# Kernel tuning notes

Measured on AMD Instinct MI355X. Metric: run time of the kernel, lower is better.

The kernel has to match this reference:

```python
import jax, jax.numpy as jnp
import numpy as np

DIM = 128      # d_msa
HEADS = 8
DH = 64        # dim_head
INNER = HEADS * DH  # 512
R = 64         # tie_attn_dim (MSA rows)
N = 512        # residues
DPAIR = 128
LN_EPS = 1e-5


def _layernorm(x, g, b):
    mu = jnp.mean(x, axis=-1, keepdims=True)
    var = jnp.mean((x - mu) ** 2, axis=-1, keepdims=True)
    return (x - mu) * jax.lax.rsqrt(var + LN_EPS) * g + b


def setup_inputs() -> dict:
    key = jax.random.key(0)
    ks = jax.random.split(key, 12)
    s = 0.02
    return {
        "x": jax.random.normal(ks[0], (R, N, DIM), jnp.float32),
        "pair_bias": jax.random.normal(ks[1], (1, N, N, DPAIR), jnp.float32),
        "Wq": jax.random.normal(ks[2], (DIM, INNER), jnp.float32) * s,
        "Wkv": jax.random.normal(ks[3], (DIM, 2 * INNER), jnp.float32) * s,
        "Wo": jax.random.normal(ks[4], (INNER, DIM), jnp.float32) * s,
        "bo": jnp.zeros((DIM,), jnp.float32),
        "ln_g": jnp.ones((DPAIR,), jnp.float32),
        "ln_b": jnp.zeros((DPAIR,), jnp.float32),
        "Wpair": jax.random.normal(ks[5], (DPAIR, HEADS), jnp.float32) * s,
        "Wsq": jax.random.normal(ks[6], (DIM, DIM), jnp.float32) * s,
        "bsq": jnp.zeros((DIM,), jnp.float32),
        "Wsk": jax.random.normal(ks[7], (DIM, DIM), jnp.float32) * s,
        "bsk": jnp.zeros((DIM,), jnp.float32),
        "tie_attn_dim": R,
    }


def reference(x, pair_bias, Wq, Wkv, Wo, bo, ln_g, ln_b, Wpair, Wsq, bsq, Wsk, bsk, tie_attn_dim):
    r = tie_attn_dim
    br, n, dim = x.shape
    b = br // r
    h, dh = HEADS, DH
    dsw = dim // h  # per-head dim inside PositionalWiseWeight

    # projections: (b*r, n, inner) -> (b, r, h, n, dh)
    q = (x @ Wq).reshape(b, r, n, h, dh).transpose(0, 1, 3, 2, 4)
    kv = x @ Wkv
    k, v = jnp.split(kv, 2, axis=-1)
    k = k.reshape(b, r, n, h, dh).transpose(0, 1, 3, 2, 4)
    v = v.reshape(b, r, n, h, dh).transpose(0, 1, 3, 2, 4)

    # soft tied row weights (PositionalWiseWeight): w[b, i(pos), h, r]
    m = x.reshape(b, r, n, dim)
    sq = (m[:, :1] @ Wsq + bsq).reshape(b, 1, n, h, dsw).transpose(0, 2, 3, 1, 4)  # b n h 1 d
    sk = (m @ Wsk + bsk).reshape(b, r, n, h, dsw).transpose(0, 2, 3, 1, 4)          # b n h r d
    wlog = jnp.einsum('bnhud,bnhrd->bnhr', sq, sk) / np.float32(np.sqrt(dsw))
    w = jax.nn.softmax(wlog, axis=-1)  # softmax over rows r

    # tied-row attention logits with soft weights
    scale = np.float32(dh) ** -0.5
    dots = jnp.einsum('bihr,brhid,brhjd->bhij', w, q, k) * scale

    # pair bias: LayerNorm + Linear(dim_pair -> heads), broadcast into logits
    pb = _layernorm(pair_bias, ln_g, ln_b) @ Wpair  # (b, i, j, h)
    dots = dots + pb.transpose(0, 3, 1, 2)

    attn = jax.nn.softmax(dots, axis=-1)  # (b, h, i, j)

    out = jnp.einsum('bhij,brhjd->brhid', attn, v)           # (b, r, h, n, dh)
    out = out.transpose(0, 1, 3, 2, 4).reshape(br, n, h * dh)
    out = out @ Wo + bo                                       # (b*r, n, dim)
    return out.reshape(1, br, n, dim)
```

## Files before the change

### kernel.cpp

```cpp
#include <hip/hip_runtime.h>
#include <hip/hip_bf16.h>

typedef unsigned short u16;
typedef unsigned int u32;
typedef __attribute__((ext_vector_type(8))) short short8;
typedef __attribute__((ext_vector_type(4))) float floatx4;

__device__ inline float bf2f(u16 u) { union { u32 i; float f; } v; v.i = ((u32)u) << 16; return v.f; }
__device__ inline u16 f2bf(float f) {
    union { float f; u32 i; } v; v.f = f;
    u32 lsb = (v.i >> 16) & 1u;
    v.i += 0x7fffu + lsb;
    return (u16)(v.i >> 16);
}

__device__ inline void ld8(u16* dst, const float* src) {
    const float4 a = *(const float4*)src;
    const float4 b = *(const float4*)(src + 4);
    uint4 q;
    q.x = (u32)f2bf(a.x) | ((u32)f2bf(a.y) << 16);
    q.y = (u32)f2bf(a.z) | ((u32)f2bf(a.w) << 16);
    q.z = (u32)f2bf(b.x) | ((u32)f2bf(b.y) << 16);
    q.w = (u32)f2bf(b.z) | ((u32)f2bf(b.w) << 16);
    *(uint4*)dst = q;
}

__device__ inline void async16(u16* ldst, const u16* gsrc) {
    __builtin_amdgcn_global_load_lds((const __attribute__((address_space(1))) u32*)gsrc,
                                     (__attribute__((address_space(3))) u32*)ldst, 16, 0, 0);
}

template <int BM, int BN, class Epi>
__global__ __launch_bounds__(256) void gemm_nt(const u16* __restrict__ A, const u16* __restrict__ B,
                                               long sAz, long sBz, int lda, int ldb, int K, int zlog, Epi epi)
{
    constexpr int AELE = BM * 32, BELE = BN * 32;
    constexpr int IA = BM / 64, IB = BN / 64;
    __shared__ __align__(16) u16 lds[2 * (AELE + BELE)];
    const int tid  = threadIdx.x;
    const int lane = tid & 63;
    const int wave = tid >> 6;
    const int z    = blockIdx.z;
    const int zh   = z >> zlog;
    const int zk   = z & ((1 << zlog) - 1);
    const long row0 = (long)blockIdx.y * BM;
    const long col0 = (long)blockIdx.x * BN;
    const u16* Ab = A + (long)zh * sAz + row0 * lda + (long)zk * K;
    const u16* Bb = B + (long)zh * sBz + col0 * ldb + (long)zk * K;
    constexpr int WM = BM / 2, WN = BN / 2, TM = WM / 16, TN = WN / 16;
    const int wm = (wave >> 1) * WM;
    const int wn = (wave & 1) * WN;
    const int l15 = lane & 15;
    const int quad = lane >> 4;
    const int swz = (l15 >> 1) & 3;

    floatx4 acc[TM][TN];
#pragma unroll
    for (int i = 0; i < TM; i++)
#pragma unroll
        for (int j = 0; j < TN; j++) acc[i][j] = (floatx4){0.f, 0.f, 0.f, 0.f};

    auto stage = [&](int buf, int k0) {
        u16* base = lds + buf * (AELE + BELE);
#pragma unroll
        for (int i = 0; i < IA; i++) {
            int s = wave * (IA * 64) + i * 64 + lane;
            int r = s >> 2, c = (s & 3) ^ ((r >> 1) & 3);
            async16(base + (wave * (IA * 64) + i * 64) * 8, Ab + (long)r * lda + k0 + c * 8);
        }
        u16* bbase = base + AELE;
#pragma unroll
        for (int i = 0; i < IB; i++) {
            int s = wave * (IB * 64) + i * 64 + lane;
            int r = s >> 2, c = (s & 3) ^ ((r >> 1) & 3);
            async16(bbase + (wave * (IB * 64) + i * 64) * 8, Bb + (long)r * ldb + k0 + c * 8);
        }
    };

    stage(0, 0);
    const int nIter = K >> 5;
    for (int ki = 0; ki < nIter; ki++) {
        const int cur = ki & 1;
        __syncthreads();
        if (ki + 1 < nIter) stage(1 - cur, (ki + 1) << 5);
        const u16* As = lds + cur * (AELE + BELE);
        const u16* Bs = As + AELE;
        short8 af[TM], bfr[TN];
#pragma unroll
        for (int t = 0; t < TM; t++)
            af[t] = *(const short8*)(As + (wm + t * 16 + l15) * 32 + (quad ^ swz) * 8);
#pragma unroll
        for (int t = 0; t < TN; t++)
            bfr[t] = *(const short8*)(Bs + (wn + t * 16 + l15) * 32 + (quad ^ swz) * 8);
#pragma unroll
        for (int i = 0; i < TM; i++)
#pragma unroll
            for (int j = 0; j < TN; j++)
                acc[i][j] = __builtin_amdgcn_mfma_f32_16x16x32_bf16(af[i], bfr[j], acc[i][j], 0, 0, 0);
    }
#pragma unroll
    for (int i = 0; i < TM; i++)
#pragma unroll
        for (int j = 0; j < TN; j++)
#pragma unroll
            for (int r = 0; r < 4; r++) {
                int row = (int)row0 + wm + i * 16 + quad * 4 + r;
                int col = (int)col0 + wn + j * 16 + l15;
                epi(zh, row, col, acc[i][j][r]);
            }
}

struct EpiBiasBF {
    u16* C; const float* bias; int ldc;
    __device__ void operator()(int, int row, int col, float v) const {
        C[(long)row * ldc + col] = f2bf(v + bias[col]);
    }
};
struct EpiQ {
    u16* Qw; const float* w;
    __device__ void operator()(int, int row, int col, float v) const {
        int r = row >> 9, i = row & 511, h = col >> 6, d = col & 63;
        float s = w[((long)(i * 8 + h)) * 64 + r] * 0.125f;
        Qw[(long)h * 2097152 + (long)i * 4096 + r * 64 + d] = f2bf(v * s);
    }
};
struct EpiKV {
    u16* Kp; u16* Vp;
    __device__ void operator()(int, int row, int col, float v) const {
        int r = row >> 9, j = row & 511, d = col & 63;
        u16 val = f2bf(v);
        if (col < 512) Kp[(long)(col >> 6) * 2097152 + (long)j * 4096 + r * 64 + d] = val;
        else           Vp[(long)((col - 512) >> 6) * 2097152 + (long)j * 4096 + r * 64 + d] = val;
    }
};
struct EpiDotsAtomic {
    float* pbdots;
    __device__ void operator()(int zh, int row, int col, float v) const {
        atomicAdd(pbdots + (long)zh * 262144 + (long)row * 512 + col, v);
    }
};
struct EpiPV {
    u16* O2;
    __device__ void operator()(int zh, int row, int col, float v) const {
        int r = col >> 6, d = col & 63;
        O2[((long)r * 512 + row) * 512 + zh * 64 + d] = f2bf(v);
    }
};
struct EpiOut {
    float* out; const float* bo;
    __device__ void operator()(int, int row, int col, float v) const {
        out[(long)row * 128 + col] = v + bo[col];
    }
};

__global__ __launch_bounds__(256) void f2bf_kernel(const float* __restrict__ src, u16* __restrict__ dst)
{
    long i = ((long)blockIdx.x * 256 + threadIdx.x) * 8;
    ld8(dst + i, src + i);
}

__global__ __launch_bounds__(256) void transpose_to_bf16(const float* __restrict__ src, u16* __restrict__ dst,
                                                         int R, int C)
{
    __shared__ u16 t[32][33];
    int c0 = blockIdx.x * 32, r0 = blockIdx.y * 32;
    int tx = threadIdx.x, ty = threadIdx.y;
#pragma unroll
    for (int i = 0; i < 32; i += 8) t[ty + i][tx] = f2bf(src[(long)(r0 + ty + i) * C + c0 + tx]);
    __syncthreads();
#pragma unroll
    for (int i = 0; i < 32; i += 8) dst[(long)(c0 + ty + i) * R + r0 + tx] = t[tx][ty + i];
}

__global__ __launch_bounds__(256) void transpose64(const u16* __restrict__ src, u16* __restrict__ dst,
                                                   long ss, long ds, int R, int C)
{
    __shared__ __align__(16) u16 t[64][72];
    const u16* s = src + (long)blockIdx.z * ss;
    u16* d = dst + (long)blockIdx.z * ds;
    int c0 = blockIdx.x * 64, r0 = blockIdx.y * 64;
    int tid = threadIdx.x;
    int row = tid >> 3, ch = tid & 7;
#pragma unroll
    for (int p = 0; p < 2; p++) {
        int r = row + p * 32;
        *(uint4*)&t[r][ch * 8] = *(const uint4*)(s + (long)(r0 + r) * C + c0 + ch * 8);
    }
    __syncthreads();
#pragma unroll
    for (int p = 0; p < 2; p++) {
        int cc = row + p * 32;
        u16 tmp[8];
#pragma unroll
        for (int j = 0; j < 8; j++) tmp[j] = t[ch * 8 + j][cc];
        *(uint4*)(d + (long)(c0 + cc) * R + r0 + ch * 8) = *(uint4*)tmp;
    }
}

__global__ __launch_bounds__(256) void rowweight_kernel(const u16* __restrict__ sk, const u16* __restrict__ sq,
                                                        float* __restrict__ w)
{
    int wid = blockIdx.x * 4 + (threadIdx.x >> 6);
    int lane = threadIdx.x & 63;
    int i = wid >> 3, h = wid & 7;
    const u16* sqp = sq + i * 128 + h * 16;
    const u16* skp = sk + ((long)lane * 512 + i) * 128 + h * 16;
    float dot = 0.f;
#pragma unroll
    for (int c = 0; c < 16; c++) dot += bf2f(sqp[c]) * bf2f(skp[c]);
    float logit = dot * 0.25f;
    float m = logit;
#pragma unroll
    for (int o = 32; o > 0; o >>= 1) m = fmaxf(m, __shfl_xor(m, o));
    float e = __expf(logit - m);
    float ssum = e;
#pragma unroll
    for (int o = 32; o > 0; o >>= 1) ssum += __shfl_xor(ssum, o);
    w[(long)wid * 64 + lane] = e / ssum;
}

__global__ __launch_bounds__(256) void pbprep_kernel(const float* __restrict__ g, const float* __restrict__ b,
                                                     const float* __restrict__ Wp, float* __restrict__ Wg,
                                                     float* __restrict__ SB)
{
    int tid = threadIdx.x;
    for (int t = tid; t < 1024; t += 256) Wg[t] = g[t >> 3] * Wp[t];
    if (tid < 16) {
        int h = tid & 7;
        const float* src = (tid < 8) ? g : b;
        float s = 0.f;
        for (int c = 0; c < 128; c++) s += src[c] * Wp[c * 8 + h];
        SB[tid] = s;
    }
}

__global__ __launch_bounds__(256) void pb_kernel(const float* __restrict__ pair, const float* __restrict__ Wg,
                                                 const float* __restrict__ SB, float* __restrict__ pb)
{
    __shared__ __align__(16) float Ls[64 * 132];
    __shared__ float sWg[1024];
    __shared__ float sSB[16];
    int tid = threadIdx.x;
    for (int t = tid; t < 1024; t += 256) sWg[t] = Wg[t];
    if (tid < 16) sSB[tid] = SB[tid];
    long base = (long)blockIdx.x * 8192;
    const float4* src = (const float4*)(pair + base);
#pragma unroll
    for (int k = 0; k < 8; k++) {
        int e = tid + k * 256;
        float4 v = src[e];
        int r = e >> 5, c = (e & 31) << 2;
        *(float4*)(&Ls[r * 132 + c]) = v;
    }
    __syncthreads();
    int r = tid >> 2, sub = tid & 3;
    const float* row = &Ls[r * 132];
    float sum = 0.f, sqs = 0.f;
#pragma unroll
    for (int k = 0; k < 8; k++) {
        float4 v = *(const float4*)(&row[sub * 32 + k * 4]);
        sum += v.x + v.y + v.z + v.w;
        sqs += v.x * v.x + v.y * v.y + v.z * v.z + v.w * v.w;
    }
    sum += __shfl_xor(sum, 1); sqs += __shfl_xor(sqs, 1);
    sum += __shfl_xor(sum, 2); sqs += __shfl_xor(sqs, 2);
    float mu = sum * (1.f / 128.f);
    float var = sqs * (1.f / 128.f) - mu * mu;
    float rstd = rsqrtf(var + 1e-5f);
    int h0 = sub * 2;
    float a0 = 0.f, a1 = 0.f;
#pragma unroll
    for (int k = 0; k < 32; k++) {
        float4 v = *(const float4*)(&row[k * 4]);
        int c = k * 4;
        a0 += v.x * sWg[c * 8 + h0]     + v.y * sWg[(c + 1) * 8 + h0]
            + v.z * sWg[(c + 2) * 8 + h0] + v.w * sWg[(c + 3) * 8 + h0];
        a1 += v.x * sWg[c * 8 + h0 + 1]     + v.y * sWg[(c + 1) * 8 + h0 + 1]
            + v.z * sWg[(c + 2) * 8 + h0 + 1] + v.w * sWg[(c + 3) * 8 + h0 + 1];
    }
    long idx = (long)blockIdx.x * 64 + r;
    pb[(long)h0 * 262144 + idx]       = rstd * (a0 - mu * sSB[h0])     + sSB[8 + h0];
    pb[(long)(h0 + 1) * 262144 + idx] = rstd * (a1 - mu * sSB[h0 + 1]) + sSB[8 + h0 + 1];
}

__global__ __launch_bounds__(256) void softmax_kernel(const float* __restrict__ dots, u16* __restrict__ attn)
{
    int row = blockIdx.x * 4 + (threadIdx.x >> 6);
    int lane = threadIdx.x & 63;
    const float* dp = dots + (long)row * 512;
    float v[8];
#pragma unroll
    for (int k = 0; k < 8; k++) v[k] = dp[k * 64 + lane];
    float m = v[0];
#pragma unroll
    for (int k = 1; k < 8; k++) m = fmaxf(m, v[k]);
#pragma unroll
    for (int o = 32; o > 0; o >>= 1) m = fmaxf(m, __shfl_xor(m, o));
    float s = 0.f;
#pragma unroll
    for (int k = 0; k < 8; k++) { v[k] = __expf(v[k] - m); s += v[k]; }
#pragma unroll
    for (int o = 32; o > 0; o >>= 1) s += __shfl_xor(s, o);
    float inv = 1.f / s;
    u16* ap = attn + (long)row * 512;
#pragma unroll
    for (int k = 0; k < 8; k++) ap[k * 64 + lane] = f2bf(v[k] * inv);
}

extern "C" void kernel_launch(void* const* d_in, const int* in_sizes, int n_in,
                              void* d_out, int out_size, void* d_ws, size_t ws_size,
                              hipStream_t stream)
{
    const float* x    = (const float*)d_in[0];
    const float* pair = (const float*)d_in[1];
    const float* Wq   = (const float*)d_in[2];
    const float* Wkv  = (const float*)d_in[3];
    const float* Wo   = (const float*)d_in[4];
    const float* bo   = (const float*)d_in[5];
    const float* lng  = (const float*)d_in[6];
    const float* lnb  = (const float*)d_in[7];
    const float* Wp   = (const float*)d_in[8];
    const float* Wsq  = (const float*)d_in[9];
    const float* bsq  = (const float*)d_in[10];
    const float* Wsk  = (const float*)d_in[11];
    const float* bsk  = (const float*)d_in[12];
    float* out = (float*)d_out;

    char* ws = (char*)d_ws;
    size_t off = 0;
    auto alloc = [&](size_t bytes) -> char* {
        char* p = ws + off; off += (bytes + 255) & ~(size_t)255; return p;
    };
    u16* WqT  = (u16*)alloc(512 * 128 * 2);
    u16* WkvT = (u16*)alloc(1024 * 128 * 2);
    u16* WskT = (u16*)alloc(128 * 128 * 2);
    u16* WsqT = (u16*)alloc(128 * 128 * 2);
    u16* WoT  = (u16*)alloc(128 * 512 * 2);
    u16* xbf  = (u16*)alloc((size_t)32768 * 128 * 2);
    u16* sk   = (u16*)alloc((size_t)32768 * 128 * 2);
    u16* sq   = (u16*)alloc(512 * 128 * 2);
    float* w  = (float*)alloc((size_t)4096 * 64 * 4);
    float* Wg = (float*)alloc(1024 * 4);
    float* SB = (float*)alloc(16 * 4);
    u16* bufA = (u16*)alloc((size_t)8 * 512 * 4096 * 2);
    u16* bufB = (u16*)alloc((size_t)8 * 512 * 4096 * 2);
    u16* Vt   = (u16*)alloc((size_t)8 * 4096 * 512 * 2);
    float* pbd = (float*)alloc((size_t)8 * 512 * 512 * 4);
    u16* attn = sk;

    dim3 blk(256);
    dim3 tb(32, 8);

    f2bf_kernel<<<dim3(2048), blk, 0, stream>>>(x, xbf);
    pbprep_kernel<<<dim3(1), blk, 0, stream>>>(lng, lnb, Wp, Wg, SB);

    transpose_to_bf16<<<dim3(16, 4, 1), tb, 0, stream>>>(Wq,  WqT,  128, 512);
    transpose_to_bf16<<<dim3(32, 4, 1), tb, 0, stream>>>(Wkv, WkvT, 128, 1024);
    transpose_to_bf16<<<dim3(4, 4, 1),  tb, 0, stream>>>(Wsk, WskT, 128, 128);
    transpose_to_bf16<<<dim3(4, 4, 1),  tb, 0, stream>>>(Wsq, WsqT, 128, 128);
    transpose_to_bf16<<<dim3(4, 16, 1), tb, 0, stream>>>(Wo,  WoT,  512, 128);

    gemm_nt<64, 128, EpiBiasBF><<<dim3(1, 512, 1), blk, 0, stream>>>(
        xbf, WskT, 0, 0, 128, 128, 128, 0, EpiBiasBF{sk, bsk, 128});
    gemm_nt<64, 128, EpiBiasBF><<<dim3(1, 8, 1), blk, 0, stream>>>(
        xbf, WsqT, 0, 0, 128, 128, 128, 0, EpiBiasBF{sq, bsq, 128});
    rowweight_kernel<<<dim3(1024), blk, 0, stream>>>(sk, sq, w);

    gemm_nt<128, 128, EpiKV><<<dim3(8, 256, 1), blk, 0, stream>>>(
        xbf, WkvT, 0, 0, 128, 128, 128, 0, EpiKV{bufB, bufA});
    transpose64<<<dim3(64, 8, 8), blk, 0, stream>>>(bufA, Vt, 2097152, 2097152, 512, 4096);

    gemm_nt<128, 128, EpiQ><<<dim3(4, 256, 1), blk, 0, stream>>>(
        xbf, WqT, 0, 0, 128, 128, 128, 0, EpiQ{bufA, w});

    pb_kernel<<<dim3(4096), blk, 0, stream>>>(pair, Wg, SB, pbd);

    gemm_nt<128, 128, EpiDotsAtomic><<<dim3(4, 4, 64), blk, 0, stream>>>(
        bufA, bufB, 2097152, 2097152, 4096, 4096, 512, 3, EpiDotsAtomic{pbd});

    softmax_kernel<<<dim3(1024), blk, 0, stream>>>(pbd, attn);

    gemm_nt<128, 128, EpiPV><<<dim3(32, 4, 8), blk, 0, stream>>>(
        attn, Vt, 262144, 2097152, 512, 512, 512, 0, EpiPV{bufB});

    gemm_nt<64, 128, EpiOut><<<dim3(1, 512, 1), blk, 0, stream>>>(
        bufB, WoT, 0, 0, 512, 512, 512, 0, EpiOut{out, bo});
}
```

Baseline: 431.5 us.

## Replace split-K atomic accumulation of dots with partial buffers reduced in softmax

The tied-row QK^T GEMM previously split K=4096 into 8 chunks and accumulated with float atomicAdd into the pair-bias buffer. It now splits into 4 chunks: chunk 0 adds in place into the pair-bias buffer, and chunks 1-3 write plain stores to separate partial buffers. The softmax kernel sums those partials while loading each row. This trades contended atomics for extra workspace and extra read traffic in the softmax, and halves the grid of the dots GEMM, which lowers parallelism. If the workspace is too small, the code falls back to the old atomic path.

```diff
diff --git a/kernel.cpp b/kernel.cpp
--- a/kernel.cpp
+++ b/kernel.cpp
@@ -106,19 +106,19 @@
             for (int r = 0; r < 4; r++) {
                 int row = (int)row0 + wm + i * 16 + quad * 4 + r;
                 int col = (int)col0 + wn + j * 16 + l15;
-                epi(zh, row, col, acc[i][j][r]);
+                epi(zh, zk, row, col, acc[i][j][r]);
             }
 }
 
 struct EpiBiasBF {
     u16* C; const float* bias; int ldc;
-    __device__ void operator()(int, int row, int col, float v) const {
+    __device__ void operator()(int, int, int row, int col, float v) const {
         C[(long)row * ldc + col] = f2bf(v + bias[col]);
     }
 };
 struct EpiQ {
     u16* Qw; const float* w;
-    __device__ void operator()(int, int row, int col, float v) const {
+    __device__ void operator()(int, int, int row, int col, float v) const {
         int r = row >> 9, i = row & 511, h = col >> 6, d = col & 63;
         float s = w[((long)(i * 8 + h)) * 64 + r] * 0.125f;
         Qw[(long)h * 2097152 + (long)i * 4096 + r * 64 + d] = f2bf(v * s);
@@ -126,7 +126,7 @@
 };
 struct EpiKV {
     u16* Kp; u16* Vp;
-    __device__ void operator()(int, int row, int col, float v) const {
+    __device__ void operator()(int, int, int row, int col, float v) const {
         int r = row >> 9, j = row & 511, d = col & 63;
         u16 val = f2bf(v);
         if (col < 512) Kp[(long)(col >> 6) * 2097152 + (long)j * 4096 + r * 64 + d] = val;
@@ -135,20 +135,28 @@
 };
 struct EpiDotsAtomic {
     float* pbdots;
-    __device__ void operator()(int zh, int row, int col, float v) const {
+    __device__ void operator()(int zh, int, int row, int col, float v) const {
         atomicAdd(pbdots + (long)zh * 262144 + (long)row * 512 + col, v);
+    }
+};
+struct EpiDotsPart {
+    float* pbd; float* parts;
+    __device__ void operator()(int zh, int zk, int row, int col, float v) const {
+        long idx = (long)zh * 262144 + (long)row * 512 + col;
+        if (zk == 0) pbd[idx] += v;
+        else         parts[(long)(zk - 1) * 2097152 + idx] = v;
     }
 };
 struct EpiPV {
     u16* O2;
-    __device__ void operator()(int zh, int row, int col, float v) const {
+    __device__ void operator()(int zh, int, int row, int col, float v) const {
         int r = col >> 6, d = col & 63;
         O2[((long)r * 512 + row) * 512 + zh * 64 + d] = f2bf(v);
     }
 };
 struct EpiOut {
     float* out; const float* bo;
-    __device__ void operator()(int, int row, int col, float v) const {
+    __device__ void operator()(int, int, int row, int col, float v) const {
         out[(long)row * 128 + col] = v + bo[col];
     }
 };
@@ -283,14 +291,22 @@
     pb[(long)(h0 + 1) * 262144 + idx] = rstd * (a1 - mu * sSB[h0 + 1]) + sSB[8 + h0 + 1];
 }
 
-__global__ __launch_bounds__(256) void softmax_kernel(const float* __restrict__ dots, u16* __restrict__ attn)
+__global__ __launch_bounds__(256) void softmax_kernel(const float* __restrict__ dots,
+                                                      const float* __restrict__ parts, int np,
+                                                      u16* __restrict__ attn)
 {
     int row = blockIdx.x * 4 + (threadIdx.x >> 6);
     int lane = threadIdx.x & 63;
-    const float* dp = dots + (long)row * 512;
+    long base = (long)row * 512;
+    const float* dp = dots + base;
     float v[8];
 #pragma unroll
     for (int k = 0; k < 8; k++) v[k] = dp[k * 64 + lane];
+    for (int t = 0; t < np; t++) {
+        const float* pp = parts + (long)t * 2097152 + base;
+#pragma unroll
+        for (int k = 0; k < 8; k++) v[k] += pp[k * 64 + lane];
+    }
     float m = v[0];
 #pragma unroll
     for (int k = 1; k < 8; k++) m = fmaxf(m, v[k]);
@@ -346,6 +362,8 @@
     u16* bufB = (u16*)alloc((size_t)8 * 512 * 4096 * 2);
     u16* Vt   = (u16*)alloc((size_t)8 * 4096 * 512 * 2);
     float* pbd = (float*)alloc((size_t)8 * 512 * 512 * 4);
+    float* parts = (float*)alloc((size_t)3 * 2097152 * 4);
+    const bool useParts = (off <= ws_size);
     u16* attn = sk;
 
     dim3 blk(256);
@@ -375,10 +393,15 @@
 
     pb_kernel<<<dim3(4096), blk, 0, stream>>>(pair, Wg, SB, pbd);
 
-    gemm_nt<128, 128, EpiDotsAtomic><<<dim3(4, 4, 64), blk, 0, stream>>>(
-        bufA, bufB, 2097152, 2097152, 4096, 4096, 512, 3, EpiDotsAtomic{pbd});
-
-    softmax_kernel<<<dim3(1024), blk, 0, stream>>>(pbd, attn);
+    if (useParts) {
+        gemm_nt<128, 128, EpiDotsPart><<<dim3(4, 4, 32), blk, 0, stream>>>(
+            bufA, bufB, 2097152, 2097152, 4096, 4096, 1024, 2, EpiDotsPart{pbd, parts});
+        softmax_kernel<<<dim3(1024), blk, 0, stream>>>(pbd, parts, 3, attn);
+    } else {
+        gemm_nt<128, 128, EpiDotsAtomic><<<dim3(4, 4, 64), blk, 0, stream>>>(
+            bufA, bufB, 2097152, 2097152, 4096, 4096, 512, 3, EpiDotsAtomic{pbd});
+        softmax_kernel<<<dim3(1024), blk, 0, stream>>>(pbd, pbd, 0, attn);
+    }
 
     gemm_nt<128, 128, EpiPV><<<dim3(32, 4, 8), blk, 0, stream>>>(
         attn, Vt, 262144, 2097152, 512, 512, 512, 0, EpiPV{bufB});
```

Measured after the change: 422.6 us. 2.1% less time.
